# Performance work log

Measured on AMD Instinct MI355X. Metric: run time of the kernel, lower is better.

Reference implementation:

```python
import jax, jax.numpy as jnp
import numpy as np

N_NODES = 100000
N_EDGES = 1600000
HID = 128
EDGE_DIM = 32
GN_EPS = 1e-5


def setup_inputs() -> dict:
    key = jax.random.key(0)
    ks = jax.random.split(key, 8)
    s = 0.05
    return {
        "x": jax.random.normal(ks[0], (N_NODES, HID), jnp.float32),
        "edge_index": jax.random.randint(ks[1], (2, N_EDGES), 0, N_NODES, jnp.int64),
        "edge_attr": jax.random.normal(ks[2], (N_EDGES, EDGE_DIM), jnp.float32),
        "edge_lin_W": jax.random.normal(ks[3], (EDGE_DIM, HID), jnp.float32) * s,
        "edge_lin_b": jnp.zeros((HID,), jnp.float32),
        "mlp_W1": jax.random.normal(ks[4], (HID, HID), jnp.float32) * s,
        "mlp_b1": jnp.zeros((HID,), jnp.float32),
        "mlp_W2": jax.random.normal(ks[5], (HID, HID), jnp.float32) * s,
        "mlp_b2": jnp.zeros((HID,), jnp.float32),
        "gn_weight": jnp.ones((HID,), jnp.float32),
        "gn_bias": jnp.zeros((HID,), jnp.float32),
        "gn_mean_scale": jnp.ones((HID,), jnp.float32),
    }


def reference(x, edge_index, edge_attr, edge_lin_W, edge_lin_b,
              mlp_W1, mlp_b1, mlp_W2, mlp_b2,
              gn_weight, gn_bias, gn_mean_scale):
    src, dst = edge_index[0], edge_index[1]
    # GINEConv message: ReLU(x_j + Lin(edge_attr)), sum-aggregated at dst
    e = edge_attr @ edge_lin_W + edge_lin_b            # [E, HID]
    msg = jax.nn.relu(x[src] + e)                      # [E, HID]
    agg = jax.ops.segment_sum(msg, dst, num_segments=x.shape[0])  # [N, HID]
    # update MLP on (1+eps)*x + agg, eps = 0
    h = agg + x
    h = jax.nn.relu(h @ mlp_W1 + mlp_b1) @ mlp_W2 + mlp_b2
    # GraphNorm with batch=None -> single graph: global node stats
    mean = jnp.mean(h, axis=0, keepdims=True)          # [1, HID]
    sub = h - gn_mean_scale * mean
    var = jnp.mean(sub * sub, axis=0, keepdims=True)
    out = gn_weight * sub / jnp.sqrt(var + GN_EPS) + gn_bias
    # final ReLU; dropout is identity at eval
    return jax.nn.relu(out)
```

## Files before the change

kernel.cpp:

```cpp
#include <hip/hip_runtime.h>
#include <stdint.h>

#define HID 128
#define EDIM 32

typedef __attribute__((ext_vector_type(8))) short bf16x8;
typedef __attribute__((ext_vector_type(4))) float f4_t;

static __device__ __forceinline__ unsigned short f2bf(float f) {
  union { float f; unsigned int u; } v; v.f = f;
  return (unsigned short)((v.u + 0x7fffu + ((v.u >> 16) & 1u)) >> 16);
}

static __device__ __forceinline__ float bf2f(short s) {
  union { unsigned int u; float f; } v;
  v.u = ((unsigned int)(unsigned short)s) << 16;
  return v.f;
}

static __device__ __forceinline__ void atomAddF(float* p, float v) {
#if defined(__gfx950__) || defined(__gfx942__) || defined(__gfx90a__)
  unsafeAtomicAdd(p, v);
#else
  atomicAdd(p, v);
#endif
}

__global__ __launch_bounds__(256) void hist_xperm(const int* __restrict__ ei,
                                                  const float* __restrict__ x,
                                                  unsigned int* __restrict__ counts,
                                                  unsigned short* __restrict__ xPerm,
                                                  int nE, int nNodes, int doPerm) {
  int tid = blockIdx.x * blockDim.x + threadIdx.x;
  const int stride = gridDim.x * blockDim.x;
  for (int i = tid; i < nE; i += stride) atomicAdd(&counts[ei[nE + i]], 1u);
  if (doPerm) {
    const int nCh = nNodes * 16;
    for (int j = tid; j < nCh; j += stride) {
      const int node = j >> 4, g = j & 15;
      const float* xp = x + (size_t)node * HID + g;
      bf16x8 o;
#pragma unroll
      for (int k = 0; k < 8; ++k) o[k] = (short)f2bf(xp[k * 16]);
      *(bf16x8*)(xPerm + (size_t)node * HID + g * 8) = o;
    }
  }
}

__global__ __launch_bounds__(1024) void chunk_sum(const unsigned int* __restrict__ counts,
                                                  unsigned int* __restrict__ chunkSum, int N) {
  __shared__ unsigned int wsum[16];
  const int tid = threadIdx.x;
  const int i = blockIdx.x * 1024 + tid;
  unsigned int v = (i < N) ? counts[i] : 0u;
#pragma unroll
  for (int d = 1; d < 64; d <<= 1) v += (unsigned int)__shfl_xor((int)v, d);
  if ((tid & 63) == 0) wsum[tid >> 6] = v;
  __syncthreads();
  if (tid < 16) {
    unsigned int t = wsum[tid];
#pragma unroll
    for (int d = 1; d < 16; d <<= 1) t += (unsigned int)__shfl_xor((int)t, d);
    if (tid == 0) chunkSum[blockIdx.x] = t;
  }
}

__global__ __launch_bounds__(256) void scan_chunks(const unsigned int* __restrict__ chunkSum,
                                                   unsigned int* __restrict__ chunkOff,
                                                   unsigned int* __restrict__ offsets,
                                                   int nChunks, int N) {
  __shared__ unsigned int wsum[4];
  const int tid = threadIdx.x, lane = tid & 63, w = tid >> 6;
  unsigned int v = (tid < nChunks) ? chunkSum[tid] : 0u;
  unsigned int s = v;
#pragma unroll
  for (int d = 1; d < 64; d <<= 1) {
    unsigned int t = (unsigned int)__shfl_up((int)s, d);
    if (lane >= d) s += t;
  }
  if (lane == 63) wsum[w] = s;
  __syncthreads();
  unsigned int wOff = 0;
  for (int k = 0; k < w; ++k) wOff += wsum[k];
  if (tid < nChunks) chunkOff[tid] = wOff + s - v;
  if (tid == nChunks - 1) offsets[N] = wOff + s;
}

__global__ __launch_bounds__(1024) void scan_local(const unsigned int* __restrict__ counts,
                                                   const unsigned int* __restrict__ chunkOff,
                                                   unsigned int* __restrict__ offsets,
                                                   unsigned int* __restrict__ cursors, int N) {
  __shared__ unsigned int wsum[16];
  const int tid = threadIdx.x, lane = tid & 63, w = tid >> 6;
  const int i = blockIdx.x * 1024 + tid;
  unsigned int v = (i < N) ? counts[i] : 0u;
  unsigned int s = v;
#pragma unroll
  for (int d = 1; d < 64; d <<= 1) {
    unsigned int t = (unsigned int)__shfl_up((int)s, d);
    if (lane >= d) s += t;
  }
  if (lane == 63) wsum[w] = s;
  __syncthreads();
  unsigned int wOff = 0;
  for (int k = 0; k < w; ++k) wOff += wsum[k];
  if (i < N) {
    const unsigned int ex = chunkOff[blockIdx.x] + wOff + (s - v);
    offsets[i] = ex;
    cursors[i] = ex;
  }
}

__global__ __launch_bounds__(256) void scatter_conv(const int* __restrict__ ei,
                                                    const float* __restrict__ ea,
                                                    unsigned int* __restrict__ cursors,
                                                    unsigned int* __restrict__ sortedSrc,
                                                    unsigned short* __restrict__ eaSorted,
                                                    int nE) {
  const int lane = threadIdx.x & 63;
  const int q = lane & 3;
  int t = blockIdx.x * blockDim.x + threadIdx.x;
  const int eStride = (gridDim.x * blockDim.x) >> 2;
  for (int e = t >> 2; e < nE; e += eStride) {
    unsigned int pos = 0;
    if (q == 0) {
      const int d = ei[nE + e];
      pos = atomicAdd(&cursors[d], 1u);
      sortedSrc[pos] = (unsigned int)ei[e];
    }
    pos = (unsigned int)__shfl((int)pos, lane & ~3);
    const f4_t* ap = (const f4_t*)(ea + (size_t)e * EDIM + q * 8);
    f4_t a0 = __builtin_nontemporal_load(ap);
    f4_t a1 = __builtin_nontemporal_load(ap + 1);
    bf16x8 o;
#pragma unroll
    for (int k = 0; k < 4; ++k) { o[k] = (short)f2bf(a0[k]); o[k + 4] = (short)f2bf(a1[k]); }
    *(bf16x8*)(eaSorted + (size_t)pos * EDIM + q * 8) = o;
  }
}

__global__ __launch_bounds__(256) void scatter_min(const int* __restrict__ ei,
                                                   unsigned int* __restrict__ cursors,
                                                   unsigned int* __restrict__ sortedEid,
                                                   unsigned int* __restrict__ sortedSrc,
                                                   int nE) {
  int i = blockIdx.x * blockDim.x + threadIdx.x;
  const int stride = gridDim.x * blockDim.x;
  for (; i < nE; i += stride) {
    const int d = ei[nE + i];
    const unsigned int pos = atomicAdd(&cursors[d], 1u);
    sortedEid[pos] = (unsigned int)i;
    sortedSrc[pos] = (unsigned int)ei[i];
  }
}

template <int BF16H>
__global__ __launch_bounds__(256) void agg_pair(
    const float* __restrict__ x, const unsigned short* __restrict__ xPerm,
    const unsigned short* __restrict__ eaSorted, const unsigned int* __restrict__ sortedSrc,
    const float* __restrict__ W, const float* __restrict__ bias,
    const unsigned int* __restrict__ offsets, float* __restrict__ h,
    unsigned short* __restrict__ hBf, int nNodes, int nPairs) {
  const int lane = threadIdx.x & 63;
  const int l15 = lane & 15;
  const int lq  = lane >> 4;

  bf16x8 Wf[8];
  float bv[8];
#pragma unroll
  for (int nt = 0; nt < 8; ++nt) {
#pragma unroll
    for (int j = 0; j < 8; ++j)
      Wf[nt][j] = (short)f2bf(W[(8 * lq + j) * HID + 16 * nt + l15]);
    bv[nt] = bias[16 * nt + l15];
  }

  int waveId = blockIdx.x * 4 + ((int)threadIdx.x >> 6);
  const int nWaves = gridDim.x * 4;

  auto LOADT = [&](unsigned int b, unsigned int end, bf16x8& af, bf16x8* xg) {
    const unsigned int sA = b + (unsigned int)l15;
    if (sA < end)
      af = __builtin_nontemporal_load((const bf16x8*)(eaSorted + (size_t)sA * EDIM + lq * 8));
    else
      af = bf16x8{0, 0, 0, 0, 0, 0, 0, 0};
#pragma unroll
    for (int r = 0; r < 4; ++r) {
      unsigned int sl = b + (unsigned int)(lq * 4 + r);
      unsigned int cl = sl < end ? sl : end - 1;
      const unsigned int src = sortedSrc[cl];
      xg[r] = *(const bf16x8*)(xPerm + (size_t)src * HID + l15 * 8);
    }
  };

  for (int p = waveId; p < nPairs; p += nWaves) {
    const int nA = p * 2;
    const int nB = (nA + 1 < nNodes) ? nA + 1 : nA;
    unsigned int bA = offsets[nA];
    const unsigned int eA = offsets[nA + 1];
    unsigned int bB = offsets[nB];
    const unsigned int eB = offsets[nB + 1];

    float accA[8] = {0, 0, 0, 0, 0, 0, 0, 0};
    float accB[8] = {0, 0, 0, 0, 0, 0, 0, 0};

    while (bA < eA || bB < eB) {
      const bool mA = bA < eA, mB = bB < eB;
      bf16x8 afA, afB, xgA[4], xgB[4];
      if (mA) LOADT(bA, eA, afA, xgA);
      if (mB) LOADT(bB, eB, afB, xgB);

      if (mA) {
        f4_t acc[8];
#pragma unroll
        for (int nt = 0; nt < 8; ++nt) {
          f4_t c; c[0] = bv[nt]; c[1] = bv[nt]; c[2] = bv[nt]; c[3] = bv[nt];
          acc[nt] = __builtin_amdgcn_mfma_f32_16x16x32_bf16(afA, Wf[nt], c, 0, 0, 0);
        }
#pragma unroll
        for (int r = 0; r < 4; ++r) {
          if (bA + (unsigned int)(lq * 4 + r) < eA) {
#pragma unroll
            for (int nt = 0; nt < 8; ++nt)
              accA[nt] += fmaxf(acc[nt][r] + bf2f(xgA[r][nt]), 0.f);
          }
        }
        bA += 16;
      }

      if (mB) {
        f4_t acc[8];
#pragma unroll
        for (int nt = 0; nt < 8; ++nt) {
          f4_t c; c[0] = bv[nt]; c[1] = bv[nt]; c[2] = bv[nt]; c[3] = bv[nt];
          acc[nt] = __builtin_amdgcn_mfma_f32_16x16x32_bf16(afB, Wf[nt], c, 0, 0, 0);
        }
#pragma unroll
        for (int r = 0; r < 4; ++r) {
          if (bB + (unsigned int)(lq * 4 + r) < eB) {
#pragma unroll
            for (int nt = 0; nt < 8; ++nt)
              accB[nt] += fmaxf(acc[nt][r] + bf2f(xgB[r][nt]), 0.f);
          }
        }
        bB += 16;
      }
    }

#pragma unroll
    for (int nt = 0; nt < 8; ++nt) {
      accA[nt] += __shfl_xor(accA[nt], 16);
      accA[nt] += __shfl_xor(accA[nt], 32);
      accB[nt] += __shfl_xor(accB[nt], 16);
      accB[nt] += __shfl_xor(accB[nt], 32);
    }

    const int c0 = 32 * lq + l15;
    const size_t rowA = (size_t)nA * HID;
    const size_t rowB = (size_t)nB * HID;
    if (BF16H) {
      const unsigned int xvA = *(const unsigned int*)(xPerm + rowA + l15 * 8 + 2 * lq);
      const unsigned int xvB = *(const unsigned int*)(xPerm + rowB + l15 * 8 + 2 * lq);
      hBf[rowA + c0]      = f2bf(accA[2 * lq]     + bf2f((short)(xvA & 0xffffu)));
      hBf[rowA + c0 + 16] = f2bf(accA[2 * lq + 1] + bf2f((short)(xvA >> 16)));
      hBf[rowB + c0]      = f2bf(accB[2 * lq]     + bf2f((short)(xvB & 0xffffu)));
      hBf[rowB + c0 + 16] = f2bf(accB[2 * lq + 1] + bf2f((short)(xvB >> 16)));
    } else {
      h[rowA + c0]      = accA[2 * lq]     + x[rowA + c0];
      h[rowA + c0 + 16] = accA[2 * lq + 1] + x[rowA + c0 + 16];
      h[rowB + c0]      = accB[2 * lq]     + x[rowB + c0];
      h[rowB + c0 + 16] = accB[2 * lq + 1] + x[rowB + c0 + 16];
    }
  }
}

__global__ __launch_bounds__(256) void agg_fb(
    const float* __restrict__ x, const float* __restrict__ ea,
    const float* __restrict__ W, const float* __restrict__ bias,
    const unsigned int* __restrict__ offsets, const unsigned int* __restrict__ sortedEid,
    const unsigned int* __restrict__ sortedSrc, float* __restrict__ h, int nNodes) {
  const int lane = threadIdx.x & 63;
  const int l15 = lane & 15;
  const int lq  = lane >> 4;

  bf16x8 Wf[8];
  float bv[8];
#pragma unroll
  for (int nt = 0; nt < 8; ++nt) {
#pragma unroll
    for (int j = 0; j < 8; ++j)
      Wf[nt][j] = (short)f2bf(W[(8 * lq + j) * HID + 16 * nt + l15]);
    bv[nt] = bias[16 * nt + l15];
  }

  int waveId = blockIdx.x * 4 + ((int)threadIdx.x >> 6);
  const int nWaves = gridDim.x * 4;

  for (int n = waveId; n < nNodes; n += nWaves) {
    const unsigned int beg = offsets[n];
    const unsigned int end = offsets[n + 1];
    float accv[8] = {0, 0, 0, 0, 0, 0, 0, 0};

    for (unsigned int base = beg; base < end; base += 16) {
      bf16x8 af = {0, 0, 0, 0, 0, 0, 0, 0};
      const unsigned int slotA = base + (unsigned int)l15;
      if (slotA < end) {
        const unsigned int eidA = sortedEid[slotA];
        const float* ap = ea + (size_t)eidA * EDIM + 8 * lq;
        f4_t a0 = *(const f4_t*)ap;
        f4_t a1 = *(const f4_t*)(ap + 4);
#pragma unroll
        for (int j = 0; j < 4; ++j) { af[j] = (short)f2bf(a0[j]); af[j + 4] = (short)f2bf(a1[j]); }
      }
      f4_t acc[8];
#pragma unroll
      for (int nt = 0; nt < 8; ++nt) {
        f4_t c; c[0] = bv[nt]; c[1] = bv[nt]; c[2] = bv[nt]; c[3] = bv[nt];
        acc[nt] = __builtin_amdgcn_mfma_f32_16x16x32_bf16(af, Wf[nt], c, 0, 0, 0);
      }
#pragma unroll
      for (int r = 0; r < 4; ++r) {
        const unsigned int slot = base + (unsigned int)(lq * 4 + r);
        if (slot < end) {
          const int s = (int)sortedSrc[slot];
          const float* xp = x + (size_t)s * HID + l15;
#pragma unroll
          for (int nt = 0; nt < 8; ++nt)
            accv[nt] += fmaxf(acc[nt][r] + xp[nt * 16], 0.f);
        }
      }
    }

#pragma unroll
    for (int nt = 0; nt < 8; ++nt) {
      accv[nt] += __shfl_xor(accv[nt], 16);
      accv[nt] += __shfl_xor(accv[nt], 32);
    }
    const int c0 = 32 * lq + l15;
    const size_t rowOff = (size_t)n * HID;
    h[rowOff + c0]      = accv[2 * lq]     + x[rowOff + c0];
    h[rowOff + c0 + 16] = accv[2 * lq + 1] + x[rowOff + c0 + 16];
  }
}

template <int BF16H>
__global__ __launch_bounds__(256) void node_kernel(
    float* __restrict__ hF, unsigned short* __restrict__ hBf,
    const float* __restrict__ W1, const float* __restrict__ b1,
    const float* __restrict__ W2, const float* __restrict__ b2,
    float* __restrict__ stats, int nNodes, int nTiles) {
  __shared__ unsigned short sW1[128 * 128];
  __shared__ unsigned short sW2[128 * 128];
  __shared__ unsigned short sH1[4][16 * 128];

  for (int idx = threadIdx.x; idx < 128 * 128; idx += 256) {
    int n = idx & 127, k = idx >> 7;
    int off = n * 128 + ((((k >> 3) ^ (n & 15))) << 3) + (k & 7);
    sW1[off] = f2bf(W1[k * HID + n]);
    sW2[off] = f2bf(W2[k * HID + n]);
  }
  __syncthreads();

  const int lane = threadIdx.x & 63;
  const int l15 = lane & 15, lq = lane >> 4;
  const int wv = threadIdx.x >> 6;
  unsigned short* hb = &sH1[wv][0];

  float b1v[8], b2v[8];
#pragma unroll
  for (int nt = 0; nt < 8; ++nt) { b1v[nt] = b1[nt * 16 + l15]; b2v[nt] = b2[nt * 16 + l15]; }
  float ssum[8] = {0, 0, 0, 0, 0, 0, 0, 0};
  float ssq[8]  = {0, 0, 0, 0, 0, 0, 0, 0};

  int waveId = blockIdx.x * 4 + wv;
  const int nWaves = gridDim.x * 4;

  for (int tile = waveId; tile < nTiles; tile += nWaves) {
    const int r0 = tile << 4;
    int rr = r0 + l15; if (rr >= nNodes) rr = nNodes - 1;

    bf16x8 af[4];
    if (BF16H) {
      const unsigned short* hp = hBf + (size_t)rr * HID;
#pragma unroll
      for (int kt = 0; kt < 4; ++kt)
        af[kt] = *(const bf16x8*)(hp + kt * 32 + 8 * lq);
    } else {
      const float* hp = hF + (size_t)rr * HID;
#pragma unroll
      for (int kt = 0; kt < 4; ++kt) {
        const int k0 = kt * 32 + 8 * lq;
        f4_t u0 = *(const f4_t*)(hp + k0);
        f4_t u1 = *(const f4_t*)(hp + k0 + 4);
#pragma unroll
        for (int j = 0; j < 4; ++j) {
          af[kt][j]     = (short)f2bf(u0[j]);
          af[kt][j + 4] = (short)f2bf(u1[j]);
        }
      }
    }

    f4_t acc[8];
#pragma unroll
    for (int nt = 0; nt < 8; ++nt) {
      f4_t c; c[0] = b1v[nt]; c[1] = b1v[nt]; c[2] = b1v[nt]; c[3] = b1v[nt];
#pragma unroll
      for (int kt = 0; kt < 4; ++kt) {
        bf16x8 wf = *(const bf16x8*)&sW1[(nt * 16 + l15) * 128 + ((((kt * 4 + lq) ^ l15)) << 3)];
        c = __builtin_amdgcn_mfma_f32_16x16x32_bf16(af[kt], wf, c, 0, 0, 0);
      }
      acc[nt] = c;
    }

#pragma unroll
    for (int nt = 0; nt < 8; ++nt) {
      const int ghi = 2 * nt + (l15 >> 3);
#pragma unroll
      for (int r = 0; r < 4; ++r) {
        const int row = lq * 4 + r;
        hb[row * 128 + ((ghi ^ (row & 15)) << 3) + (l15 & 7)] = f2bf(fmaxf(acc[nt][r], 0.f));
      }
    }
    asm volatile("s_waitcnt lgkmcnt(0)" ::: "memory");
    __builtin_amdgcn_sched_barrier(0);

    bf16x8 af2[4];
#pragma unroll
    for (int kt = 0; kt < 4; ++kt)
      af2[kt] = *(const bf16x8*)&hb[l15 * 128 + ((((kt * 4 + lq) ^ l15)) << 3)];

    f4_t acc2[8];
#pragma unroll
    for (int nt = 0; nt < 8; ++nt) {
      f4_t c; c[0] = b2v[nt]; c[1] = b2v[nt]; c[2] = b2v[nt]; c[3] = b2v[nt];
#pragma unroll
      for (int kt = 0; kt < 4; ++kt) {
        bf16x8 wf = *(const bf16x8*)&sW2[(nt * 16 + l15) * 128 + ((((kt * 4 + lq) ^ l15)) << 3)];
        c = __builtin_amdgcn_mfma_f32_16x16x32_bf16(af2[kt], wf, c, 0, 0, 0);
      }
      acc2[nt] = c;
    }

#pragma unroll
    for (int nt = 0; nt < 8; ++nt) {
#pragma unroll
      for (int r = 0; r < 4; ++r) {
        const int row = r0 + lq * 4 + r;
        if (row < nNodes) {
          float v = acc2[nt][r];
          if (BF16H) hBf[(size_t)row * HID + nt * 16 + l15] = f2bf(v);
          else       hF[(size_t)row * HID + nt * 16 + l15] = v;
          ssum[nt] += v; ssq[nt] += v * v;
        }
      }
    }
  }

#pragma unroll
  for (int nt = 0; nt < 8; ++nt) {
    float a = ssum[nt], b = ssq[nt];
    a += __shfl_xor(a, 16); b += __shfl_xor(b, 16);
    a += __shfl_xor(a, 32); b += __shfl_xor(b, 32);
    if (lq == 0) {
      atomAddF(&stats[nt * 16 + l15], a);
      atomAddF(&stats[HID + nt * 16 + l15], b);
    }
  }
}

__global__ void norm_prep(float* __restrict__ stats, const float* __restrict__ gw,
                          const float* __restrict__ gb, const float* __restrict__ gs,
                          int nNodes) {
  int c = threadIdx.x;
  if (c < HID) {
    float invN = 1.f / (float)nNodes;
    float m   = stats[c] * invN;
    float msq = stats[HID + c] * invN;
    float s   = gs[c];
    float var = msq - (2.f * s - s * s) * m * m;
    float A = gw[c] * rsqrtf(var + 1e-5f);
    float B = gb[c] - A * s * m;
    stats[2 * HID + c] = A;
    stats[3 * HID + c] = B;
  }
}

__global__ __launch_bounds__(256) void norm_bf(const float* __restrict__ stats,
                                               const unsigned short* __restrict__ hBf,
                                               float* __restrict__ out, int total8) {
  const float* A = stats + 2 * HID;
  const float* B = stats + 3 * HID;
  int i = blockIdx.x * blockDim.x + threadIdx.x;
  const int stride = gridDim.x * blockDim.x;
  for (; i < total8; i += stride) {
    const int cg = (i & 15) * 8;
    bf16x8 hv = *(const bf16x8*)(hBf + (size_t)i * 8);
    f4_t a0 = *(const f4_t*)(A + cg), a1 = *(const f4_t*)(A + cg + 4);
    f4_t b0 = *(const f4_t*)(B + cg), b1 = *(const f4_t*)(B + cg + 4);
    f4_t o0, o1;
#pragma unroll
    for (int j = 0; j < 4; ++j) {
      o0[j] = fmaxf(fmaf(bf2f(hv[j]), a0[j], b0[j]), 0.f);
      o1[j] = fmaxf(fmaf(bf2f(hv[j + 4]), a1[j], b1[j]), 0.f);
    }
    f4_t* op = (f4_t*)(out + (size_t)i * 8);
    op[0] = o0; op[1] = o1;
  }
}

__global__ __launch_bounds__(256) void norm_kernel(const float* __restrict__ stats,
                                                   float* __restrict__ out, int total4) {
  const f4_t* A4 = (const f4_t*)(stats + 2 * HID);
  const f4_t* B4 = (const f4_t*)(stats + 3 * HID);
  int i = blockIdx.x * blockDim.x + threadIdx.x;
  const int stride = gridDim.x * blockDim.x;
  for (; i < total4; i += stride) {
    const int cg = i & 31;
    f4_t h = ((const f4_t*)out)[i];
    f4_t a = A4[cg], b = B4[cg];
    f4_t o;
#pragma unroll
    for (int j = 0; j < 4; ++j) o[j] = fmaxf(fmaf(h[j], a[j], b[j]), 0.f);
    ((f4_t*)out)[i] = o;
  }
}

extern "C" void kernel_launch(void* const* d_in, const int* in_sizes, int n_in,
                              void* d_out, int out_size, void* d_ws, size_t ws_size,
                              hipStream_t stream) {
  const float* x  = (const float*)d_in[0];
  const int*   ei = (const int*)d_in[1];
  const float* ea = (const float*)d_in[2];
  const float* eW = (const float*)d_in[3];
  const float* eb = (const float*)d_in[4];
  const float* W1 = (const float*)d_in[5];
  const float* b1 = (const float*)d_in[6];
  const float* W2 = (const float*)d_in[7];
  const float* b2 = (const float*)d_in[8];
  const float* gw = (const float*)d_in[9];
  const float* gb = (const float*)d_in[10];
  const float* gs = (const float*)d_in[11];
  float* out = (float*)d_out;

  const int nNodes = in_sizes[0] / HID;
  const int nE     = in_sizes[1] / 2;

  char* w = (char*)d_ws;
  const size_t offStats   = 0;
  const size_t offCounts  = 2048;
  const size_t offCursors = offCounts  + (size_t)nNodes * 4;
  const size_t offOffsets = offCursors + (size_t)nNodes * 4;
  const size_t offChunk   = offOffsets + (((size_t)(nNodes + 1) * 4 + 63) & ~63ull);
  const size_t offSS      = (offChunk + 2048 + 63) & ~63ull;
  const size_t offEaS     = offSS + (size_t)nE * 4;
  const size_t offXP      = offEaS + (size_t)nE * EDIM * 2;
  const size_t needFlat   = offXP + (size_t)nNodes * HID * 2;
  const size_t offHBf     = needFlat;
  const size_t needBf     = offHBf + (size_t)nNodes * HID * 2;

  float* stats            = (float*)(w + offStats);
  unsigned int* counts    = (unsigned int*)(w + offCounts);
  unsigned int* cursors   = (unsigned int*)(w + offCursors);
  unsigned int* offsets   = (unsigned int*)(w + offOffsets);
  unsigned int* chunkSum  = (unsigned int*)(w + offChunk);
  unsigned int* chunkOff  = (unsigned int*)(w + offChunk + 1024);
  unsigned int* sortedSrc = (unsigned int*)(w + offSS);
  unsigned int* sortedEid = (unsigned int*)(w + offEaS);
  unsigned short* eaSorted= (unsigned short*)(w + offEaS);
  unsigned short* xPerm   = (unsigned short*)(w + offXP);
  unsigned short* hBf     = (unsigned short*)(w + offHBf);

  const int mode = (ws_size >= needBf) ? 2 : (ws_size >= needFlat ? 1 : 0);

  hipMemsetAsync(d_ws, 0, offCursors, stream);

  hist_xperm<<<2048, 256, 0, stream>>>(ei, x, counts, xPerm, nE, nNodes, mode >= 1);

  const int nChunks = (nNodes + 1023) / 1024;
  chunk_sum<<<nChunks, 1024, 0, stream>>>(counts, chunkSum, nNodes);
  scan_chunks<<<1, 256, 0, stream>>>(chunkSum, chunkOff, offsets, nChunks, nNodes);
  scan_local<<<nChunks, 1024, 0, stream>>>(counts, chunkOff, offsets, cursors, nNodes);

  const int nTiles = (nNodes + 15) >> 4;

  if (mode >= 1) {
    scatter_conv<<<4096, 256, 0, stream>>>(ei, ea, cursors, sortedSrc, eaSorted, nE);
    const int nPairs = (nNodes + 1) / 2;
    const int blocks = (nPairs + 7) / 8;
    if (mode == 2) {
      agg_pair<1><<<blocks, 256, 0, stream>>>(x, xPerm, eaSorted, sortedSrc, eW, eb,
                                              offsets, out, hBf, nNodes, nPairs);
      node_kernel<1><<<512, 256, 0, stream>>>(nullptr, hBf, W1, b1, W2, b2, stats,
                                              nNodes, nTiles);
      norm_prep<<<1, 128, 0, stream>>>(stats, gw, gb, gs, nNodes);
      norm_bf<<<2048, 256, 0, stream>>>(stats, hBf, out, nNodes * (HID / 8));
    } else {
      agg_pair<0><<<blocks, 256, 0, stream>>>(x, xPerm, eaSorted, sortedSrc, eW, eb,
                                              offsets, out, hBf, nNodes, nPairs);
      node_kernel<0><<<512, 256, 0, stream>>>(out, nullptr, W1, b1, W2, b2, stats,
                                              nNodes, nTiles);
      norm_prep<<<1, 128, 0, stream>>>(stats, gw, gb, gs, nNodes);
      norm_kernel<<<2048, 256, 0, stream>>>(stats, out, nNodes * (HID / 4));
    }
  } else {
    scatter_min<<<1024, 256, 0, stream>>>(ei, cursors, sortedEid, sortedSrc, nE);
    agg_fb<<<8192, 256, 0, stream>>>(x, ea, eW, eb, offsets, sortedEid, sortedSrc, out, nNodes);
    node_kernel<0><<<512, 256, 0, stream>>>(out, nullptr, W1, b1, W2, b2, stats,
                                            nNodes, nTiles);
    norm_prep<<<1, 128, 0, stream>>>(stats, gw, gb, gs, nNodes);
    norm_kernel<<<2048, 256, 0, stream>>>(stats, out, nNodes * (HID / 4));
  }
}
```

Before: 419.7 us.

## Split fused two-layer node MLP into separate kernels for the bf16 path

On the bf16 path, the node MLP that ran both matmuls in one kernel is split into two kernels. The first writes the ReLU hidden layer to a bf16 scratch buffer that reuses the sorted edge-attribute region. Each kernel now keeps only one 32KB weight matrix in LDS and launches 1024 blocks instead of 512, aiming for higher occupancy. The cost is an extra kernel launch plus a full write and read of the N×128 bf16 intermediate through global memory.

Measured after the change: 488.2 us. 1.16x slower.

```diff
diff --git a/kernel.cpp b/kernel.cpp
--- a/kernel.cpp
+++ b/kernel.cpp
@@ -343,10 +343,134 @@
   }
 }
 
-template <int BF16H>
+__global__ __launch_bounds__(256) void node1_bf(
+    const unsigned short* __restrict__ hBf, const float* __restrict__ W1,
+    const float* __restrict__ b1, unsigned short* __restrict__ h1Bf,
+    int nNodes, int nTiles) {
+  __shared__ unsigned short sW1[128 * 128];
+  for (int idx = threadIdx.x; idx < 128 * 128; idx += 256) {
+    int n = idx & 127, k = idx >> 7;
+    int off = n * 128 + ((((k >> 3) ^ (n & 15))) << 3) + (k & 7);
+    sW1[off] = f2bf(W1[k * HID + n]);
+  }
+  __syncthreads();
+
+  const int lane = threadIdx.x & 63;
+  const int l15 = lane & 15, lq = lane >> 4;
+  float b1v[8];
+#pragma unroll
+  for (int nt = 0; nt < 8; ++nt) b1v[nt] = b1[nt * 16 + l15];
+
+  int waveId = blockIdx.x * 4 + ((int)threadIdx.x >> 6);
+  const int nWaves = gridDim.x * 4;
+
+  for (int tile = waveId; tile < nTiles; tile += nWaves) {
+    const int r0 = tile << 4;
+    int rr = r0 + l15; if (rr >= nNodes) rr = nNodes - 1;
+
+    bf16x8 af[4];
+    const unsigned short* hp = hBf + (size_t)rr * HID;
+#pragma unroll
+    for (int kt = 0; kt < 4; ++kt)
+      af[kt] = *(const bf16x8*)(hp + kt * 32 + 8 * lq);
+
+    f4_t acc[8];
+#pragma unroll
+    for (int nt = 0; nt < 8; ++nt) {
+      f4_t c; c[0] = b1v[nt]; c[1] = b1v[nt]; c[2] = b1v[nt]; c[3] = b1v[nt];
+#pragma unroll
+      for (int kt = 0; kt < 4; ++kt) {
+        bf16x8 wf = *(const bf16x8*)&sW1[(nt * 16 + l15) * 128 + ((((kt * 4 + lq) ^ l15)) << 3)];
+        c = __builtin_amdgcn_mfma_f32_16x16x32_bf16(af[kt], wf, c, 0, 0, 0);
+      }
+      acc[nt] = c;
+    }
+
+#pragma unroll
+    for (int nt = 0; nt < 8; ++nt) {
+#pragma unroll
+      for (int r = 0; r < 4; ++r) {
+        const int row = r0 + lq * 4 + r;
+        if (row < nNodes)
+          h1Bf[(size_t)row * HID + nt * 16 + l15] = f2bf(fmaxf(acc[nt][r], 0.f));
+      }
+    }
+  }
+}
+
+__global__ __launch_bounds__(256) void node2_bf(
+    const unsigned short* __restrict__ h1Bf, const float* __restrict__ W2,
+    const float* __restrict__ b2, unsigned short* __restrict__ hBf,
+    float* __restrict__ stats, int nNodes, int nTiles) {
+  __shared__ unsigned short sW2[128 * 128];
+  for (int idx = threadIdx.x; idx < 128 * 128; idx += 256) {
+    int n = idx & 127, k = idx >> 7;
+    int off = n * 128 + ((((k >> 3) ^ (n & 15))) << 3) + (k & 7);
+    sW2[off] = f2bf(W2[k * HID + n]);
+  }
+  __syncthreads();
+
+  const int lane = threadIdx.x & 63;
+  const int l15 = lane & 15, lq = lane >> 4;
+  float b2v[8];
+#pragma unroll
+  for (int nt = 0; nt < 8; ++nt) b2v[nt] = b2[nt * 16 + l15];
+  float ssum[8] = {0, 0, 0, 0, 0, 0, 0, 0};
+  float ssq[8]  = {0, 0, 0, 0, 0, 0, 0, 0};
+
+  int waveId = blockIdx.x * 4 + ((int)threadIdx.x >> 6);
+  const int nWaves = gridDim.x * 4;
+
+  for (int tile = waveId; tile < nTiles; tile += nWaves) {
+    const int r0 = tile << 4;
+    int rr = r0 + l15; if (rr >= nNodes) rr = nNodes - 1;
+
+    bf16x8 af[4];
+    const unsigned short* hp = h1Bf + (size_t)rr * HID;
+#pragma unroll
+    for (int kt = 0; kt < 4; ++kt)
+      af[kt] = *(const bf16x8*)(hp + kt * 32 + 8 * lq);
+
+    f4_t acc[8];
+#pragma unroll
+    for (int nt = 0; nt < 8; ++nt) {
+      f4_t c; c[0] = b2v[nt]; c[1] = b2v[nt]; c[2] = b2v[nt]; c[3] = b2v[nt];
+#pragma unroll
+      for (int kt = 0; kt < 4; ++kt) {
+        bf16x8 wf = *(const bf16x8*)&sW2[(nt * 16 + l15) * 128 + ((((kt * 4 + lq) ^ l15)) << 3)];
+        c = __builtin_amdgcn_mfma_f32_16x16x32_bf16(af[kt], wf, c, 0, 0, 0);
+      }
+      acc[nt] = c;
+    }
+
+#pragma unroll
+    for (int nt = 0; nt < 8; ++nt) {
+#pragma unroll
+      for (int r = 0; r < 4; ++r) {
+        const int row = r0 + lq * 4 + r;
+        if (row < nNodes) {
+          float v = acc[nt][r];
+          hBf[(size_t)row * HID + nt * 16 + l15] = f2bf(v);
+          ssum[nt] += v; ssq[nt] += v * v;
+        }
+      }
+    }
+  }
+
+#pragma unroll
+  for (int nt = 0; nt < 8; ++nt) {
+    float a = ssum[nt], b = ssq[nt];
+    a += __shfl_xor(a, 16); b += __shfl_xor(b, 16);
+    a += __shfl_xor(a, 32); b += __shfl_xor(b, 32);
+    if (lq == 0) {
+      atomAddF(&stats[nt * 16 + l15], a);
+      atomAddF(&stats[HID + nt * 16 + l15], b);
+    }
+  }
+}
+
 __global__ __launch_bounds__(256) void node_kernel(
-    float* __restrict__ hF, unsigned short* __restrict__ hBf,
-    const float* __restrict__ W1, const float* __restrict__ b1,
+    float* __restrict__ hF, const float* __restrict__ W1, const float* __restrict__ b1,
     const float* __restrict__ W2, const float* __restrict__ b2,
     float* __restrict__ stats, int nNodes, int nTiles) {
   __shared__ unsigned short sW1[128 * 128];
@@ -380,23 +504,16 @@
     int rr = r0 + l15; if (rr >= nNodes) rr = nNodes - 1;
 
     bf16x8 af[4];
-    if (BF16H) {
-      const unsigned short* hp = hBf + (size_t)rr * HID;
-#pragma unroll
-      for (int kt = 0; kt < 4; ++kt)
-        af[kt] = *(const bf16x8*)(hp + kt * 32 + 8 * lq);
-    } else {
-      const float* hp = hF + (size_t)rr * HID;
-#pragma unroll
-      for (int kt = 0; kt < 4; ++kt) {
-        const int k0 = kt * 32 + 8 * lq;
-        f4_t u0 = *(const f4_t*)(hp + k0);
-        f4_t u1 = *(const f4_t*)(hp + k0 + 4);
-#pragma unroll
-        for (int j = 0; j < 4; ++j) {
-          af[kt][j]     = (short)f2bf(u0[j]);
-          af[kt][j + 4] = (short)f2bf(u1[j]);
-        }
+    const float* hp = hF + (size_t)rr * HID;
+#pragma unroll
+    for (int kt = 0; kt < 4; ++kt) {
+      const int k0 = kt * 32 + 8 * lq;
+      f4_t u0 = *(const f4_t*)(hp + k0);
+      f4_t u1 = *(const f4_t*)(hp + k0 + 4);
+#pragma unroll
+      for (int j = 0; j < 4; ++j) {
+        af[kt][j]     = (short)f2bf(u0[j]);
+        af[kt][j + 4] = (short)f2bf(u1[j]);
       }
     }
 
@@ -448,8 +565,7 @@
         const int row = r0 + lq * 4 + r;
         if (row < nNodes) {
           float v = acc2[nt][r];
-          if (BF16H) hBf[(size_t)row * HID + nt * 16 + l15] = f2bf(v);
-          else       hF[(size_t)row * HID + nt * 16 + l15] = v;
+          hF[(size_t)row * HID + nt * 16 + l15] = v;
           ssum[nt] += v; ssq[nt] += v * v;
         }
       }
@@ -569,6 +685,7 @@
   unsigned short* eaSorted= (unsigned short*)(w + offEaS);
   unsigned short* xPerm   = (unsigned short*)(w + offXP);
   unsigned short* hBf     = (unsigned short*)(w + offHBf);
+  unsigned short* h1Bf    = (unsigned short*)(w + offEaS);
 
   const int mode = (ws_size >= needBf) ? 2 : (ws_size >= needFlat ? 1 : 0);
 
@@ -590,23 +707,21 @@
     if (mode == 2) {
       agg_pair<1><<<blocks, 256, 0, stream>>>(x, xPerm, eaSorted, sortedSrc, eW, eb,
                                               offsets, out, hBf, nNodes, nPairs);
-      node_kernel<1><<<512, 256, 0, stream>>>(nullptr, hBf, W1, b1, W2, b2, stats,
-                                              nNodes, nTiles);
+      node1_bf<<<1024, 256, 0, stream>>>(hBf, W1, b1, h1Bf, nNodes, nTiles);
+      node2_bf<<<1024, 256, 0, stream>>>(h1Bf, W2, b2, hBf, stats, nNodes, nTiles);
       norm_prep<<<1, 128, 0, stream>>>(stats, gw, gb, gs, nNodes);
       norm_bf<<<2048, 256, 0, stream>>>(stats, hBf, out, nNodes * (HID / 8));
     } else {
       agg_pair<0><<<blocks, 256, 0, stream>>>(x, xPerm, eaSorted, sortedSrc, eW, eb,
                                               offsets, out, hBf, nNodes, nPairs);
-      node_kernel<0><<<512, 256, 0, stream>>>(out, nullptr, W1, b1, W2, b2, stats,
-                                              nNodes, nTiles);
+      node_kernel<<<512, 256, 0, stream>>>(out, W1, b1, W2, b2, stats, nNodes, nTiles);
       norm_prep<<<1, 128, 0, stream>>>(stats, gw, gb, gs, nNodes);
       norm_kernel<<<2048, 256, 0, stream>>>(stats, out, nNodes * (HID / 4));
     }
   } else {
     scatter_min<<<1024, 256, 0, stream>>>(ei, cursors, sortedEid, sortedSrc, nE);
     agg_fb<<<8192, 256, 0, stream>>>(x, ea, eW, eb, offsets, sortedEid, sortedSrc, out, nNodes);
-    node_kernel<0><<<512, 256, 0, stream>>>(out, nullptr, W1, b1, W2, b2, stats,
-                                            nNodes, nTiles);
+    node_kernel<<<512, 256, 0, stream>>>(out, W1, b1, W2, b2, stats, nNodes, nTiles);
     norm_prep<<<1, 128, 0, stream>>>(stats, gw, gb, gs, nNodes);
     norm_kernel<<<2048, 256, 0, stream>>>(stats, out, nNodes * (HID / 4));
   }
```
